# Optimization experiments

Measured on AMD Instinct MI355X. Metric: run time of the kernel, lower is better.

Reference implementation:

```python
import jax, jax.numpy as jnp
import numpy as np

N = 100000      # nodes
E = 1600000     # edges (avg degree 16)
D = 64          # in_channels == conv widths == lin width
G = 64          # graphs in batch
OUT = 10        # out_channels


def setup_inputs() -> dict:
    key = jax.random.key(0)
    ks = jax.random.split(key, 20)
    s = 0.1
    inp = {
        "x": jax.random.normal(ks[0], (N, D), jnp.float32),
        "edge_index": jax.random.randint(ks[1], (2, E), 0, N, dtype=jnp.int64),
        "batch": jnp.sort(jax.random.randint(ks[2], (N,), 0, G, dtype=jnp.int64)),
    }
    k = 3
    for i in range(3):  # 3 SAGEConv layers: lin_l (Wl, bl) on aggregated, lin_r (Wr, no bias) on root
        inp[f"c{i}_Wl"] = jax.random.normal(ks[k], (D, D), jnp.float32) * s; k += 1
        inp[f"c{i}_bl"] = jnp.zeros((D,), jnp.float32)
        inp[f"c{i}_Wr"] = jax.random.normal(ks[k], (D, D), jnp.float32) * s; k += 1
    inp["l0_W"] = jax.random.normal(ks[k], (D, D), jnp.float32) * s; k += 1
    inp["l0_b"] = jnp.zeros((D,), jnp.float32)
    inp["out_W"] = jax.random.normal(ks[k], (D, OUT), jnp.float32) * s; k += 1
    inp["out_b"] = jnp.zeros((OUT,), jnp.float32)
    return inp


def reference(x, edge_index, batch,
              c0_Wl, c0_bl, c0_Wr,
              c1_Wl, c1_bl, c1_Wr,
              c2_Wl, c2_bl, c2_Wr,
              l0_W, l0_b, out_W, out_b):
    src, dst = edge_index[0], edge_index[1]
    # in-degree of each target node (mean conv aggregation), computed once
    deg = jax.ops.segment_sum(jnp.ones((E,), x.dtype), dst, num_segments=N)
    inv_deg = (1.0 / jnp.maximum(deg, 1.0))[:, None]

    def sage(h, Wl, bl, Wr):
        # gather source features, mean-aggregate at targets, then lin_l(agg) + lin_r(h)
        agg = jax.ops.segment_sum(h[src], dst, num_segments=N) * inv_deg
        return agg @ Wl + bl + h @ Wr

    h = jax.nn.relu(sage(x, c0_Wl, c0_bl, c0_Wr))
    h = jax.nn.relu(sage(h, c1_Wl, c1_bl, c1_Wr))
    h = jax.nn.relu(sage(h, c2_Wl, c2_bl, c2_Wr))

    # global mean pool over graphs
    cnt = jax.ops.segment_sum(jnp.ones((N,), h.dtype), batch, num_segments=G)
    g = jax.ops.segment_sum(h, batch, num_segments=G) / jnp.maximum(cnt, 1.0)[:, None]

    g = jax.nn.relu(g @ l0_W + l0_b)
    return g @ out_W + out_b  # [G, OUT]
```

## Files before the change

kernel.cpp:

```cpp
#include <hip/hip_runtime.h>
#include <hip/hip_fp16.h>

#define WPB 8
#define PADK 136
#define BSH 8
#define BNODES 256
#define SC_BLOCKS 256
#define HIST_BLOCKS 256
#define HSTRIDE 512

typedef _Float16 half8 __attribute__((ext_vector_type(8)));
typedef _Float16 half4v __attribute__((ext_vector_type(4)));
typedef float floatx4 __attribute__((ext_vector_type(4)));

__global__ __launch_bounds__(256) void gnn_pre(const int* __restrict__ dst,
                                               int* __restrict__ bkt_cnt, int nbkt, int E,
                                               const int* __restrict__ batch,
                                               float* __restrict__ gcnt, int N,
                                               const float4* __restrict__ xin,
                                               ushort4* __restrict__ x16o, int n4,
                                               __half* __restrict__ x16,
                                               __half* __restrict__ hA,
                                               __half* __restrict__ hB,
                                               int* __restrict__ hist_all) {
    int tid = threadIdx.x;
    if (blockIdx.x < HIST_BLOCKS) {
        __shared__ int h[512];
        __shared__ int gb[64];
        for (int i = tid; i < nbkt; i += 256) h[i] = 0;
        if (tid < 64) gb[tid] = 0;
        __syncthreads();
        const int stride = HIST_BLOCKS * 256;
        if ((E & 3) == 0) {
            const int4* dst4 = (const int4*)dst;
            int E4 = E >> 2;
            for (int e = blockIdx.x * 256 + tid; e < E4; e += stride) {
                int4 d = dst4[e];
                atomicAdd(&h[d.x >> BSH], 1);
                atomicAdd(&h[d.y >> BSH], 1);
                atomicAdd(&h[d.z >> BSH], 1);
                atomicAdd(&h[d.w >> BSH], 1);
            }
        } else {
            for (int e = blockIdx.x * 256 + tid; e < E; e += stride)
                atomicAdd(&h[dst[e] >> BSH], 1);
        }
        for (int i = blockIdx.x * 256 + tid; i < N; i += stride)
            atomicAdd(&gb[batch[i]], 1);
        __syncthreads();
        for (int i = tid; i < nbkt; i += 256) {
            int v = h[i];
            hist_all[blockIdx.x * HSTRIDE + i] = v;
            if (v) atomicAdd(&bkt_cnt[i], v);
        }
        if (tid < 64) {
            int v = gb[tid];
            if (v) atomicAdd(&gcnt[tid], (float)v);
        }
        if (blockIdx.x == 0 && tid < 64) {
            x16[(size_t)N * 64 + tid] = __ushort_as_half((unsigned short)0);
            hA[(size_t)N * 64 + tid] = __ushort_as_half((unsigned short)0);
            hB[(size_t)N * 64 + tid] = __ushort_as_half((unsigned short)0);
        }
    } else {
        int i = (blockIdx.x - HIST_BLOCKS) * 256 + tid;
        if (i < n4) {
            float4 f = xin[i];
            ushort4 o;
            o.x = __half_as_ushort(__float2half(f.x));
            o.y = __half_as_ushort(__float2half(f.y));
            o.z = __half_as_ushort(__float2half(f.z));
            o.w = __half_as_ushort(__float2half(f.w));
            x16o[i] = o;
        }
    }
}

__global__ __launch_bounds__(256) void gnn_scan2(const int* __restrict__ hist_all,
                                                 const int* __restrict__ bkt_cnt,
                                                 int* __restrict__ bkt_base,
                                                 int* __restrict__ row_ptr,
                                                 int* __restrict__ blk_base_all,
                                                 int nbkt, int N) {
    int b = blockIdx.x;
    int t = threadIdx.x, lane = t & 63, wv = t >> 6;
    __shared__ int wsum[4];
    __shared__ int red[4];
    int part = 0;
    for (int i = t; i < b; i += 256) part += bkt_cnt[i];
#pragma unroll
    for (int off = 1; off < 64; off <<= 1) part += __shfl_xor(part, off);
    if (lane == 0) red[wv] = part;
    int v = hist_all[t * HSTRIDE + b];
    int x = v;
#pragma unroll
    for (int off = 1; off < 64; off <<= 1) {
        int y = __shfl_up(x, off);
        if (lane >= off) x += y;
    }
    if (lane == 63) wsum[wv] = x;
    __syncthreads();
    int base = red[0] + red[1] + red[2] + red[3];
    int wexcl = 0;
    for (int w = 0; w < wv; w++) wexcl += wsum[w];
    blk_base_all[t * HSTRIDE + b] = base + wexcl + (x - v);
    if (t == 0) {
        bkt_base[b] = base;
        if (b == nbkt - 1) {
            int tot = base + bkt_cnt[b];
            bkt_base[nbkt] = tot;
            row_ptr[N] = tot;
        }
    }
}

__global__ __launch_bounds__(256) void gnn_bkt_scatter(const int* __restrict__ src,
                                                       const int* __restrict__ dst,
                                                       const int* __restrict__ blk_base_all,
                                                       unsigned int* __restrict__ pairs,
                                                       int E, int nbkt) {
    __shared__ int cur[512];
    int tid = threadIdx.x;
    for (int i = tid; i < nbkt; i += 256) cur[i] = blk_base_all[blockIdx.x * HSTRIDE + i];
    __syncthreads();
    const int stride = SC_BLOCKS * 256;
    if ((E & 3) == 0) {
        const int4* dst4 = (const int4*)dst;
        const int4* src4 = (const int4*)src;
        int E4 = E >> 2;
        for (int e = blockIdx.x * 256 + tid; e < E4; e += stride) {
            int4 d = dst4[e];
            int4 s = src4[e];
            int p0 = atomicAdd(&cur[d.x >> BSH], 1);
            pairs[p0] = (unsigned int)s.x | ((unsigned int)(d.x & (BNODES - 1)) << 24);
            int p1 = atomicAdd(&cur[d.y >> BSH], 1);
            pairs[p1] = (unsigned int)s.y | ((unsigned int)(d.y & (BNODES - 1)) << 24);
            int p2 = atomicAdd(&cur[d.z >> BSH], 1);
            pairs[p2] = (unsigned int)s.z | ((unsigned int)(d.z & (BNODES - 1)) << 24);
            int p3 = atomicAdd(&cur[d.w >> BSH], 1);
            pairs[p3] = (unsigned int)s.w | ((unsigned int)(d.w & (BNODES - 1)) << 24);
        }
    } else {
        for (int e = blockIdx.x * 256 + tid; e < E; e += stride) {
            int d = dst[e];
            int b = d >> BSH;
            int p = atomicAdd(&cur[b], 1);
            pairs[p] = (unsigned int)src[e] | ((unsigned int)(d & (BNODES - 1)) << 24);
        }
    }
}

__global__ __launch_bounds__(256) void gnn_bkt_csr(const unsigned int* __restrict__ pairs,
                                                   const int* __restrict__ bkt_base,
                                                   int* __restrict__ row_ptr,
                                                   float* __restrict__ inv_deg,
                                                   int* __restrict__ csr_src, int N) {
    __shared__ int hist[BNODES];
    __shared__ int excl[BNODES];
    __shared__ int cur[BNODES];
    int b = blockIdx.x;
    int base = bkt_base[b];
    int cnt = bkt_base[b + 1] - base;
    int nd0 = b << BSH;
    int tid = threadIdx.x;
    hist[tid] = 0;
    __syncthreads();
    {
        int a0 = (4 - (base & 3)) & 3;
        a0 = min(a0, cnt);
        for (int i = tid; i < a0; i += 256) atomicAdd(&hist[pairs[base + i] >> 24], 1);
        int vcnt = (cnt - a0) >> 2;
        const uint4* p4 = (const uint4*)(pairs + base + a0);
        for (int i = tid; i < vcnt; i += 256) {
            uint4 u = p4[i];
            atomicAdd(&hist[u.x >> 24], 1);
            atomicAdd(&hist[u.y >> 24], 1);
            atomicAdd(&hist[u.z >> 24], 1);
            atomicAdd(&hist[u.w >> 24], 1);
        }
        for (int i = a0 + (vcnt << 2) + tid; i < cnt; i += 256)
            atomicAdd(&hist[pairs[base + i] >> 24], 1);
    }
    __syncthreads();
    if (tid < 64) {
        int carry = 0;
#pragma unroll
        for (int c = 0; c < BNODES; c += 64) {
            int v = hist[c + tid];
            int x = v;
#pragma unroll
            for (int off = 1; off < 64; off <<= 1) {
                int y = __shfl_up(x, off);
                if (tid >= off) x += y;
            }
            excl[c + tid] = carry + (x - v);
            carry += __shfl(x, 63);
        }
    }
    __syncthreads();
    {
        int node = nd0 + tid;
        if (node < N) {
            row_ptr[node] = base + excl[tid];
            int d = hist[tid];
            inv_deg[node] = 1.0f / (float)(d > 1 ? d : 1);
        }
        cur[tid] = excl[tid];
    }
    __syncthreads();
    {
        int a0 = (4 - (base & 3)) & 3;
        a0 = min(a0, cnt);
        for (int i = tid; i < a0; i += 256) {
            unsigned int u = pairs[base + i];
            int pos = atomicAdd(&cur[u >> 24], 1);
            csr_src[base + pos] = (int)(u & 0xFFFFFFu);
        }
        int vcnt = (cnt - a0) >> 2;
        const uint4* p4 = (const uint4*)(pairs + base + a0);
        for (int i = tid; i < vcnt; i += 256) {
            uint4 u = p4[i];
            int pos0 = atomicAdd(&cur[u.x >> 24], 1);
            csr_src[base + pos0] = (int)(u.x & 0xFFFFFFu);
            int pos1 = atomicAdd(&cur[u.y >> 24], 1);
            csr_src[base + pos1] = (int)(u.y & 0xFFFFFFu);
            int pos2 = atomicAdd(&cur[u.z >> 24], 1);
            csr_src[base + pos2] = (int)(u.z & 0xFFFFFFu);
            int pos3 = atomicAdd(&cur[u.w >> 24], 1);
            csr_src[base + pos3] = (int)(u.w & 0xFFFFFFu);
        }
        for (int i = a0 + (vcnt << 2) + tid; i < cnt; i += 256) {
            unsigned int u = pairs[base + i];
            int pos = atomicAdd(&cur[u >> 24], 1);
            csr_src[base + pos] = (int)(u & 0xFFFFFFu);
        }
    }
}

#define LOAD4(eReg, c0, vArr)                                  \
    _Pragma("unroll") for (int c_ = 0; c_ < 4; c_++) {         \
        int sj_ = __shfl(eReg, (c0) + c_ * 4 + quad);          \
        vArr[c_] = hin4v[(size_t)sj_ * 16 + m16];              \
    }
#define ACC4(vArr, accum)                                      \
    _Pragma("unroll") for (int c_ = 0; c_ < 4; c_++) {         \
        accum.x += (float)vArr[c_][0];                         \
        accum.y += (float)vArr[c_][1];                         \
        accum.z += (float)vArr[c_][2];                         \
        accum.w += (float)vArr[c_][3];                         \
    }

__global__ __launch_bounds__(512, 4) void gnn_sage(const __half* __restrict__ hin,
                                                   __half* __restrict__ hout,
                                                   const int* __restrict__ row_ptr,
                                                   const int* __restrict__ csr_src,
                                                   const float* __restrict__ inv_deg,
                                                   const float* __restrict__ Wl,
                                                   const float* __restrict__ bl,
                                                   const float* __restrict__ Wr, int n) {
    __shared__ _Float16 w_lds[64 * PADK];
    __shared__ _Float16 in_lds[WPB][16 * PADK];
    int tid = threadIdx.x, lane = tid & 63, wv = tid >> 6;
    for (int i = tid; i < 64 * 64; i += 512) {
        int k = i >> 6, nn = i & 63;
        w_lds[nn * PADK + k] = (_Float16)Wl[i];
        w_lds[nn * PADK + 64 + k] = (_Float16)Wr[i];
    }
    __syncthreads();
    int ngroups = (n + 15) >> 4;
    int g = blockIdx.x * WPB + wv;
    if (g >= ngroups) return;
    int m16 = lane & 15, quad = lane >> 4;
    int hf = lane >> 5, col = lane & 31;
    float bias[4];
#pragma unroll
    for (int nt = 0; nt < 4; nt++) bias[nt] = bl[nt * 16 + m16];
    _Float16* my_in = in_lds[wv];
    const unsigned* hin32 = (const unsigned*)hin;
    const half4v* hin4v = (const half4v*)hin;
    int nd0 = g << 4;
    int nclamp = n - 1 - nd0;
    int idx = nd0 + lane;
    int rr = (lane <= 16) ? row_ptr[min(idx, n)] : 0;
    float ig = (lane < 16) ? inv_deg[min(idx, n - 1)] : 0.0f;

#pragma unroll
    for (int jp = 0; jp < 8; jp++) {
        int j2 = jp << 1;
        int nd = nd0 + min(j2 + hf, nclamp);
        unsigned u = hin32[(size_t)nd * 32 + col];
        ((unsigned*)(my_in + (j2 + hf) * PADK + 64))[col] = u;
    }

    int ef[16];
#pragma unroll
    for (int j = 0; j < 16; j++) {
        int jj = min(j, nclamp);
        int s0 = __shfl(rr, jj), s1 = __shfl(rr, jj + 1);
        int cb = min(64, s1 - s0);
        ef[j] = (lane < cb) ? csr_src[s0 + lane] : n;
    }

#pragma unroll
    for (int jp = 0; jp < 8; jp++) {
        int j2 = jp << 1;
        int jjA = min(j2, nclamp), jjB = min(j2 + 1, nclamp);
        int s0A = __shfl(rr, jjA), s1A = __shfl(rr, jjA + 1);
        int s0B = __shfl(rr, jjB), s1B = __shfl(rr, jjB + 1);
        float idgA = __shfl(ig, jjA), idgB = __shfl(ig, jjB);
        int cbA = min(64, s1A - s0A), cbB = min(64, s1B - s0B);
        floatx4 accA = {0.f, 0.f, 0.f, 0.f};
        floatx4 accB = {0.f, 0.f, 0.f, 0.f};
        {
            half4v vA[4], vB[4];
            LOAD4(ef[j2], 0, vA);
            LOAD4(ef[j2 + 1], 0, vB);
            ACC4(vA, accA);
            ACC4(vB, accB);
        }
        if (cbA > 16) {
            half4v v0[4];
            LOAD4(ef[j2], 16, v0);
            ACC4(v0, accA);
            if (cbA > 32) { half4v v1[4]; LOAD4(ef[j2], 32, v1); ACC4(v1, accA); }
            if (cbA > 48) { half4v v2[4]; LOAD4(ef[j2], 48, v2); ACC4(v2, accA); }
        }
        if (cbB > 16) {
            half4v v0[4];
            LOAD4(ef[j2 + 1], 16, v0);
            ACC4(v0, accB);
            if (cbB > 32) { half4v v1[4]; LOAD4(ef[j2 + 1], 32, v1); ACC4(v1, accB); }
            if (cbB > 48) { half4v v2[4]; LOAD4(ef[j2 + 1], 48, v2); ACC4(v2, accB); }
        }
        for (int base_ = s0A + 64; base_ < s1A; base_ += 64) {
            int cb = min(64, s1A - base_);
            int ei = (lane < cb) ? csr_src[base_ + lane] : n;
            for (int i0 = 0; i0 < cb; i0 += 16) {
                half4v vt[4];
                LOAD4(ei, i0, vt);
                ACC4(vt, accA);
            }
        }
        for (int base_ = s0B + 64; base_ < s1B; base_ += 64) {
            int cb = min(64, s1B - base_);
            int ei = (lane < cb) ? csr_src[base_ + lane] : n;
            for (int i0 = 0; i0 < cb; i0 += 16) {
                half4v vt[4];
                LOAD4(ei, i0, vt);
                ACC4(vt, accB);
            }
        }
        accA.x += __shfl_xor(accA.x, 16); accA.y += __shfl_xor(accA.y, 16);
        accA.z += __shfl_xor(accA.z, 16); accA.w += __shfl_xor(accA.w, 16);
        accA.x += __shfl_xor(accA.x, 32); accA.y += __shfl_xor(accA.y, 32);
        accA.z += __shfl_xor(accA.z, 32); accA.w += __shfl_xor(accA.w, 32);
        accB.x += __shfl_xor(accB.x, 16); accB.y += __shfl_xor(accB.y, 16);
        accB.z += __shfl_xor(accB.z, 16); accB.w += __shfl_xor(accB.w, 16);
        accB.x += __shfl_xor(accB.x, 32); accB.y += __shfl_xor(accB.y, 32);
        accB.z += __shfl_xor(accB.z, 32); accB.w += __shfl_xor(accB.w, 32);
        if (quad == 0) {
            half4v hw;
            hw[0] = (_Float16)(accA.x * idgA);
            hw[1] = (_Float16)(accA.y * idgA);
            hw[2] = (_Float16)(accA.z * idgA);
            hw[3] = (_Float16)(accA.w * idgA);
            *(half4v*)(my_in + j2 * PADK + m16 * 4) = hw;
        } else if (quad == 1) {
            half4v hw;
            hw[0] = (_Float16)(accB.x * idgB);
            hw[1] = (_Float16)(accB.y * idgB);
            hw[2] = (_Float16)(accB.z * idgB);
            hw[3] = (_Float16)(accB.w * idgB);
            *(half4v*)(my_in + (j2 + 1) * PADK + m16 * 4) = hw;
        }
    }
    half8 afrag[4];
    const _Float16* abase = my_in + m16 * PADK + quad * 8;
#pragma unroll
    for (int ks = 0; ks < 4; ks++) afrag[ks] = *(const half8*)(abase + ks * 32);
    floatx4 accv[4];
#pragma unroll
    for (int nt = 0; nt < 4; nt++) {
        accv[nt].x = 0.f; accv[nt].y = 0.f; accv[nt].z = 0.f; accv[nt].w = 0.f;
    }
#pragma unroll
    for (int nt = 0; nt < 4; nt++) {
        const _Float16* bbase = w_lds + (nt * 16 + m16) * PADK + quad * 8;
#pragma unroll
        for (int ks = 0; ks < 4; ks++) {
            half8 bfrag = *(const half8*)(bbase + ks * 32);
            accv[nt] = __builtin_amdgcn_mfma_f32_16x16x32_f16(afrag[ks], bfrag, accv[nt], 0, 0, 0);
        }
    }
#pragma unroll
    for (int nt = 0; nt < 4; nt++) {
#pragma unroll
        for (int r = 0; r < 4; r++) {
            int node = nd0 + quad * 4 + r;
            if (node < n) {
                float v = fmaxf(accv[nt][r] + bias[nt], 0.0f);
                hout[(size_t)node * 64 + nt * 16 + m16] = __float2half(v);
            }
        }
    }
}

__global__ __launch_bounds__(512, 4) void gnn_sage_pool(const __half* __restrict__ hin,
                                                        const int* __restrict__ row_ptr,
                                                        const int* __restrict__ csr_src,
                                                        const float* __restrict__ inv_deg,
                                                        const float* __restrict__ Wl,
                                                        const float* __restrict__ bl,
                                                        const float* __restrict__ Wr,
                                                        const int* __restrict__ batch,
                                                        float* __restrict__ gsum,
                                                        const float* __restrict__ gcnt,
                                                        const float* __restrict__ l0W,
                                                        const float* __restrict__ l0b,
                                                        const float* __restrict__ outW,
                                                        const float* __restrict__ outb,
                                                        float* __restrict__ out,
                                                        unsigned int* __restrict__ done,
                                                        int G, int OUT, int n) {
    __shared__ _Float16 w_lds[64 * PADK];
    __shared__ _Float16 in_lds[WPB][16 * PADK];
    __shared__ int lastsh;
    int tid = threadIdx.x, lane = tid & 63, wv = tid >> 6;
    for (int i = tid; i < 64 * 64; i += 512) {
        int k = i >> 6, nn = i & 63;
        w_lds[nn * PADK + k] = (_Float16)Wl[i];
        w_lds[nn * PADK + 64 + k] = (_Float16)Wr[i];
    }
    __syncthreads();
    int ngroups = (n + 15) >> 4;
    int g = blockIdx.x * WPB + wv;
    int m16 = lane & 15, quad = lane >> 4;
    int hf = lane >> 5, col = lane & 31;
    const unsigned* hin32 = (const unsigned*)hin;
    const half4v* hin4v = (const half4v*)hin;
    if (g < ngroups) {
        float bias[4];
#pragma unroll
        for (int nt = 0; nt < 4; nt++) bias[nt] = bl[nt * 16 + m16];
        _Float16* my_in = in_lds[wv];
        int nd0 = g << 4;
        int nclamp = n - 1 - nd0;
        int idx = nd0 + lane;
        int rr = (lane <= 16) ? row_ptr[min(idx, n)] : 0;
        float ig = (lane < 16) ? inv_deg[min(idx, n - 1)] : 0.0f;

#pragma unroll
        for (int jp = 0; jp < 8; jp++) {
            int j2 = jp << 1;
            int nd = nd0 + min(j2 + hf, nclamp);
            unsigned u = hin32[(size_t)nd * 32 + col];
            ((unsigned*)(my_in + (j2 + hf) * PADK + 64))[col] = u;
        }

        int ef[16];
#pragma unroll
        for (int j = 0; j < 16; j++) {
            int jj = min(j, nclamp);
            int s0 = __shfl(rr, jj), s1 = __shfl(rr, jj + 1);
            int cb = min(64, s1 - s0);
            ef[j] = (lane < cb) ? csr_src[s0 + lane] : n;
        }

#pragma unroll
        for (int jp = 0; jp < 8; jp++) {
            int j2 = jp << 1;
            int jjA = min(j2, nclamp), jjB = min(j2 + 1, nclamp);
            int s0A = __shfl(rr, jjA), s1A = __shfl(rr, jjA + 1);
            int s0B = __shfl(rr, jjB), s1B = __shfl(rr, jjB + 1);
            float idgA = __shfl(ig, jjA), idgB = __shfl(ig, jjB);
            int cbA = min(64, s1A - s0A), cbB = min(64, s1B - s0B);
            floatx4 accA = {0.f, 0.f, 0.f, 0.f};
            floatx4 accB = {0.f, 0.f, 0.f, 0.f};
            {
                half4v vA[4], vB[4];
                LOAD4(ef[j2], 0, vA);
                LOAD4(ef[j2 + 1], 0, vB);
                ACC4(vA, accA);
                ACC4(vB, accB);
            }
            if (cbA > 16) {
                half4v v0[4];
                LOAD4(ef[j2], 16, v0);
                ACC4(v0, accA);
                if (cbA > 32) { half4v v1[4]; LOAD4(ef[j2], 32, v1); ACC4(v1, accA); }
                if (cbA > 48) { half4v v2[4]; LOAD4(ef[j2], 48, v2); ACC4(v2, accA); }
            }
            if (cbB > 16) {
                half4v v0[4];
                LOAD4(ef[j2 + 1], 16, v0);
                ACC4(v0, accB);
                if (cbB > 32) { half4v v1[4]; LOAD4(ef[j2 + 1], 32, v1); ACC4(v1, accB); }
                if (cbB > 48) { half4v v2[4]; LOAD4(ef[j2 + 1], 48, v2); ACC4(v2, accB); }
            }
            for (int base_ = s0A + 64; base_ < s1A; base_ += 64) {
                int cb = min(64, s1A - base_);
                int ei = (lane < cb) ? csr_src[base_ + lane] : n;
                for (int i0 = 0; i0 < cb; i0 += 16) {
                    half4v vt[4];
                    LOAD4(ei, i0, vt);
                    ACC4(vt, accA);
                }
            }
            for (int base_ = s0B + 64; base_ < s1B; base_ += 64) {
                int cb = min(64, s1B - base_);
                int ei = (lane < cb) ? csr_src[base_ + lane] : n;
                for (int i0 = 0; i0 < cb; i0 += 16) {
                    half4v vt[4];
                    LOAD4(ei, i0, vt);
                    ACC4(vt, accB);
                }
            }
            accA.x += __shfl_xor(accA.x, 16); accA.y += __shfl_xor(accA.y, 16);
            accA.z += __shfl_xor(accA.z, 16); accA.w += __shfl_xor(accA.w, 16);
            accA.x += __shfl_xor(accA.x, 32); accA.y += __shfl_xor(accA.y, 32);
            accA.z += __shfl_xor(accA.z, 32); accA.w += __shfl_xor(accA.w, 32);
            accB.x += __shfl_xor(accB.x, 16); accB.y += __shfl_xor(accB.y, 16);
            accB.z += __shfl_xor(accB.z, 16); accB.w += __shfl_xor(accB.w, 16);
            accB.x += __shfl_xor(accB.x, 32); accB.y += __shfl_xor(accB.y, 32);
            accB.z += __shfl_xor(accB.z, 32); accB.w += __shfl_xor(accB.w, 32);
            if (quad == 0) {
                half4v hw;
                hw[0] = (_Float16)(accA.x * idgA);
                hw[1] = (_Float16)(accA.y * idgA);
                hw[2] = (_Float16)(accA.z * idgA);
                hw[3] = (_Float16)(accA.w * idgA);
                *(half4v*)(my_in + j2 * PADK + m16 * 4) = hw;
            } else if (quad == 1) {
                half4v hw;
                hw[0] = (_Float16)(accB.x * idgB);
                hw[1] = (_Float16)(accB.y * idgB);
                hw[2] = (_Float16)(accB.z * idgB);
                hw[3] = (_Float16)(accB.w * idgB);
                *(half4v*)(my_in + (j2 + 1) * PADK + m16 * 4) = hw;
            }
        }
        half8 afrag[4];
        const _Float16* abase = my_in + m16 * PADK + quad * 8;
#pragma unroll
        for (int ks = 0; ks < 4; ks++) afrag[ks] = *(const half8*)(abase + ks * 32);
        floatx4 accv[4];
#pragma unroll
        for (int nt = 0; nt < 4; nt++) {
            accv[nt].x = 0.f; accv[nt].y = 0.f; accv[nt].z = 0.f; accv[nt].w = 0.f;
        }
#pragma unroll
        for (int nt = 0; nt < 4; nt++) {
            const _Float16* bbase = w_lds + (nt * 16 + m16) * PADK + quad * 8;
#pragma unroll
            for (int ks = 0; ks < 4; ks++) {
                half8 bfrag = *(const half8*)(bbase + ks * 32);
                accv[nt] = __builtin_amdgcn_mfma_f32_16x16x32_f16(afrag[ks], bfrag, accv[nt], 0, 0, 0);
            }
        }
        int bFirst = batch[nd0];
        int bLast = batch[min(nd0 + 15, n - 1)];
        if (bFirst == bLast && nd0 + 15 < n) {
#pragma unroll
            for (int nt = 0; nt < 4; nt++) {
                float s = fmaxf(accv[nt][0] + bias[nt], 0.0f) + fmaxf(accv[nt][1] + bias[nt], 0.0f) +
                          fmaxf(accv[nt][2] + bias[nt], 0.0f) + fmaxf(accv[nt][3] + bias[nt], 0.0f);
                s += __shfl_xor(s, 16);
                s += __shfl_xor(s, 32);
                if (quad == 0) atomicAdd(&gsum[bFirst * 64 + nt * 16 + m16], s);
            }
        } else {
#pragma unroll
            for (int nt = 0; nt < 4; nt++) {
#pragma unroll
                for (int r = 0; r < 4; r++) {
                    int node = nd0 + quad * 4 + r;
                    if (node < n) {
                        int bg = batch[node];
                        float v = fmaxf(accv[nt][r] + bias[nt], 0.0f);
                        atomicAdd(&gsum[bg * 64 + nt * 16 + m16], v);
                    }
                }
            }
        }
    }
    __syncthreads();
    if (tid == 0) {
        __threadfence();
        unsigned int old = atomicAdd(done, 1u);
        lastsh = (old == gridDim.x - 1) ? 1 : 0;
    }
    __syncthreads();
    if (lastsh) {
        float* gm = (float*)&in_lds[0][0];
        float* t2 = gm + 64 * 64;
        for (int i = tid; i < G * 64; i += 512) {
            int r = i >> 6;
            float s = atomicAdd(&gsum[i], 0.0f);
            gm[i] = s / fmaxf(gcnt[r], 1.0f);
        }
        __syncthreads();
        for (int i = tid; i < G * 64; i += 512) {
            int r = i >> 6, c = i & 63;
            float s = l0b[c];
#pragma unroll 8
            for (int k = 0; k < 64; k++) s += gm[(r << 6) + k] * l0W[(k << 6) + c];
            t2[i] = fmaxf(s, 0.0f);
        }
        __syncthreads();
        for (int i = tid; i < G * OUT; i += 512) {
            int r = i / OUT, c = i - r * OUT;
            float s = outb[c];
#pragma unroll 8
            for (int k = 0; k < 64; k++) s += t2[(r << 6) + k] * outW[k * OUT + c];
            out[i] = s;
        }
    }
}

extern "C" void kernel_launch(void* const* d_in, const int* in_sizes, int n_in,
                              void* d_out, int out_size, void* d_ws, size_t ws_size,
                              hipStream_t stream) {
    const float* x = (const float*)d_in[0];
    const int* ei = (const int*)d_in[1];
    const int* batch = (const int*)d_in[2];
    const float* Wl[3] = {(const float*)d_in[3], (const float*)d_in[6], (const float*)d_in[9]};
    const float* bl[3] = {(const float*)d_in[4], (const float*)d_in[7], (const float*)d_in[10]};
    const float* Wr[3] = {(const float*)d_in[5], (const float*)d_in[8], (const float*)d_in[11]};
    const float* l0W = (const float*)d_in[12];
    const float* l0b = (const float*)d_in[13];
    const float* outW = (const float*)d_in[14];
    const float* outb = (const float*)d_in[15];

    int N = in_sizes[2];
    int E = in_sizes[1] / 2;
    int OUT = 10;
    int G = out_size / OUT;
    const int* src = ei;
    const int* dst = ei + E;
    int NBKT = (N + BNODES - 1) >> BSH;

    char* ws = (char*)d_ws;
    size_t off = 0;
    auto alloc = [&](size_t b) -> char* {
        char* p = ws + off;
        off = (off + b + 255) & ~(size_t)255;
        return p;
    };
    int* row_ptr = (int*)alloc((size_t)(N + 1) * 4);
    int* csr_src = (int*)alloc((size_t)E * 4);
    float* inv_deg = (float*)alloc((size_t)N * 4);
    size_t zoff = off;
    int* bkt_cnt = (int*)alloc((size_t)NBKT * 4);
    float* gcnt = (float*)alloc((size_t)G * 4);
    float* gsum = (float*)alloc((size_t)G * 64 * 4);
    unsigned int* done = (unsigned int*)alloc(4);
    size_t zlen = off - zoff;
    int* bkt_base = (int*)alloc((size_t)(NBKT + 1) * 4);
    int* hist_all = (int*)alloc((size_t)HIST_BLOCKS * HSTRIDE * 4);
    int* blk_base_all = (int*)alloc((size_t)HIST_BLOCKS * HSTRIDE * 4);
    unsigned int* pairs = (unsigned int*)alloc((size_t)E * 4);
    __half* x16 = (__half*)alloc((size_t)(N + 1) * 64 * 2);
    __half* hA = (__half*)alloc((size_t)(N + 1) * 64 * 2);
    __half* hB = (__half*)alloc((size_t)(N + 1) * 64 * 2);

    hipMemsetAsync(ws + zoff, 0, zlen, stream);

    int n4 = N * 64 / 4;
    int pre_blocks = HIST_BLOCKS + (n4 + 255) / 256;
    gnn_pre<<<pre_blocks, 256, 0, stream>>>(dst, bkt_cnt, NBKT, E, batch, gcnt, N,
                                            (const float4*)x, (ushort4*)x16, n4,
                                            x16, hA, hB, hist_all);
    gnn_scan2<<<NBKT, 256, 0, stream>>>(hist_all, bkt_cnt, bkt_base, row_ptr,
                                        blk_base_all, NBKT, N);
    gnn_bkt_scatter<<<SC_BLOCKS, 256, 0, stream>>>(src, dst, blk_base_all, pairs, E, NBKT);
    gnn_bkt_csr<<<NBKT, 256, 0, stream>>>(pairs, bkt_base, row_ptr, inv_deg, csr_src, N);

    int ngroups = (N + 15) >> 4;
    int sage_blocks = (ngroups + WPB - 1) / WPB;
    gnn_sage<<<sage_blocks, 512, 0, stream>>>(x16, hA, row_ptr, csr_src, inv_deg,
                                              Wl[0], bl[0], Wr[0], N);
    gnn_sage<<<sage_blocks, 512, 0, stream>>>(hA, hB, row_ptr, csr_src, inv_deg,
                                              Wl[1], bl[1], Wr[1], N);
    gnn_sage_pool<<<sage_blocks, 512, 0, stream>>>(hB, row_ptr, csr_src, inv_deg,
                                                   Wl[2], bl[2], Wr[2], batch, gsum,
                                                   gcnt, l0W, l0b, outW, outb,
                                                   (float*)d_out, done, G, OUT, N);
}
```

Baseline: 304.5 us.

## Stage bucket pairs in LDS for CSR build and split pooling head into own kernel

The bucket CSR kernel now copies each bucket's packed pairs into a 48KB shared-memory buffer during the histogram pass. The scatter pass reads them from LDS instead of re-reading global memory, and it drops the uint4-vectorized global loads. Separately, the last-block-done atomic counter and tail MLP head are removed from the final SAGE/pool kernel and moved to a separate single-block head kernel. This lets waves with no work exit early and removes the threadfence and atomic handshake. The cost is an extra kernel launch, and the large LDS buffer may lower occupancy in the CSR kernel.

```diff
diff --git a/kernel.cpp b/kernel.cpp
--- a/kernel.cpp
+++ b/kernel.cpp
@@ -8,6 +8,7 @@
 #define SC_BLOCKS 256
 #define HIST_BLOCKS 256
 #define HSTRIDE 512
+#define PSTAGE 12288
 
 typedef _Float16 half8 __attribute__((ext_vector_type(8)));
 typedef _Float16 half4v __attribute__((ext_vector_type(4)));
@@ -158,6 +159,7 @@
     __shared__ int hist[BNODES];
     __shared__ int excl[BNODES];
     __shared__ int cur[BNODES];
+    __shared__ unsigned int pstage[PSTAGE];
     int b = blockIdx.x;
     int base = bkt_base[b];
     int cnt = bkt_base[b + 1] - base;
@@ -165,22 +167,14 @@
     int tid = threadIdx.x;
     hist[tid] = 0;
     __syncthreads();
-    {
-        int a0 = (4 - (base & 3)) & 3;
-        a0 = min(a0, cnt);
-        for (int i = tid; i < a0; i += 256) atomicAdd(&hist[pairs[base + i] >> 24], 1);
-        int vcnt = (cnt - a0) >> 2;
-        const uint4* p4 = (const uint4*)(pairs + base + a0);
-        for (int i = tid; i < vcnt; i += 256) {
-            uint4 u = p4[i];
-            atomicAdd(&hist[u.x >> 24], 1);
-            atomicAdd(&hist[u.y >> 24], 1);
-            atomicAdd(&hist[u.z >> 24], 1);
-            atomicAdd(&hist[u.w >> 24], 1);
-        }
-        for (int i = a0 + (vcnt << 2) + tid; i < cnt; i += 256)
-            atomicAdd(&hist[pairs[base + i] >> 24], 1);
-    }
+    int scnt = min(cnt, PSTAGE);
+    for (int i = tid; i < scnt; i += 256) {
+        unsigned int u = pairs[base + i];
+        pstage[i] = u;
+        atomicAdd(&hist[u >> 24], 1);
+    }
+    for (int i = scnt + tid; i < cnt; i += 256)
+        atomicAdd(&hist[pairs[base + i] >> 24], 1);
     __syncthreads();
     if (tid < 64) {
         int carry = 0;
@@ -208,32 +202,15 @@
         cur[tid] = excl[tid];
     }
     __syncthreads();
-    {
-        int a0 = (4 - (base & 3)) & 3;
-        a0 = min(a0, cnt);
-        for (int i = tid; i < a0; i += 256) {
-            unsigned int u = pairs[base + i];
-            int pos = atomicAdd(&cur[u >> 24], 1);
-            csr_src[base + pos] = (int)(u & 0xFFFFFFu);
-        }
-        int vcnt = (cnt - a0) >> 2;
-        const uint4* p4 = (const uint4*)(pairs + base + a0);
-        for (int i = tid; i < vcnt; i += 256) {
-            uint4 u = p4[i];
-            int pos0 = atomicAdd(&cur[u.x >> 24], 1);
-            csr_src[base + pos0] = (int)(u.x & 0xFFFFFFu);
-            int pos1 = atomicAdd(&cur[u.y >> 24], 1);
-            csr_src[base + pos1] = (int)(u.y & 0xFFFFFFu);
-            int pos2 = atomicAdd(&cur[u.z >> 24], 1);
-            csr_src[base + pos2] = (int)(u.z & 0xFFFFFFu);
-            int pos3 = atomicAdd(&cur[u.w >> 24], 1);
-            csr_src[base + pos3] = (int)(u.w & 0xFFFFFFu);
-        }
-        for (int i = a0 + (vcnt << 2) + tid; i < cnt; i += 256) {
-            unsigned int u = pairs[base + i];
-            int pos = atomicAdd(&cur[u >> 24], 1);
-            csr_src[base + pos] = (int)(u & 0xFFFFFFu);
-        }
+    for (int i = tid; i < scnt; i += 256) {
+        unsigned int u = pstage[i];
+        int pos = atomicAdd(&cur[u >> 24], 1);
+        csr_src[base + pos] = (int)(u & 0xFFFFFFu);
+    }
+    for (int i = scnt + tid; i < cnt; i += 256) {
+        unsigned int u = pairs[base + i];
+        int pos = atomicAdd(&cur[u >> 24], 1);
+        csr_src[base + pos] = (int)(u & 0xFFFFFFu);
     }
 }
 
@@ -413,18 +390,9 @@
                                                         const float* __restrict__ bl,
                                                         const float* __restrict__ Wr,
                                                         const int* __restrict__ batch,
-                                                        float* __restrict__ gsum,
-                                                        const float* __restrict__ gcnt,
-                                                        const float* __restrict__ l0W,
-                                                        const float* __restrict__ l0b,
-                                                        const float* __restrict__ outW,
-                                                        const float* __restrict__ outb,
-                                                        float* __restrict__ out,
-                                                        unsigned int* __restrict__ done,
-                                                        int G, int OUT, int n) {
+                                                        float* __restrict__ gsum, int n) {
     __shared__ _Float16 w_lds[64 * PADK];
     __shared__ _Float16 in_lds[WPB][16 * PADK];
-    __shared__ int lastsh;
     int tid = threadIdx.x, lane = tid & 63, wv = tid >> 6;
     for (int i = tid; i < 64 * 64; i += 512) {
         int k = i >> 6, nn = i & 63;
@@ -434,186 +402,185 @@
     __syncthreads();
     int ngroups = (n + 15) >> 4;
     int g = blockIdx.x * WPB + wv;
+    if (g >= ngroups) return;
     int m16 = lane & 15, quad = lane >> 4;
     int hf = lane >> 5, col = lane & 31;
+    float bias[4];
+#pragma unroll
+    for (int nt = 0; nt < 4; nt++) bias[nt] = bl[nt * 16 + m16];
+    _Float16* my_in = in_lds[wv];
     const unsigned* hin32 = (const unsigned*)hin;
     const half4v* hin4v = (const half4v*)hin;
-    if (g < ngroups) {
-        float bias[4];
-#pragma unroll
-        for (int nt = 0; nt < 4; nt++) bias[nt] = bl[nt * 16 + m16];
-        _Float16* my_in = in_lds[wv];
-        int nd0 = g << 4;
-        int nclamp = n - 1 - nd0;
-        int idx = nd0 + lane;
-        int rr = (lane <= 16) ? row_ptr[min(idx, n)] : 0;
-        float ig = (lane < 16) ? inv_deg[min(idx, n - 1)] : 0.0f;
-
-#pragma unroll
-        for (int jp = 0; jp < 8; jp++) {
-            int j2 = jp << 1;
-            int nd = nd0 + min(j2 + hf, nclamp);
-            unsigned u = hin32[(size_t)nd * 32 + col];
-            ((unsigned*)(my_in + (j2 + hf) * PADK + 64))[col] = u;
-        }
-
-        int ef[16];
-#pragma unroll
-        for (int j = 0; j < 16; j++) {
-            int jj = min(j, nclamp);
-            int s0 = __shfl(rr, jj), s1 = __shfl(rr, jj + 1);
-            int cb = min(64, s1 - s0);
-            ef[j] = (lane < cb) ? csr_src[s0 + lane] : n;
-        }
-
-#pragma unroll
-        for (int jp = 0; jp < 8; jp++) {
-            int j2 = jp << 1;
-            int jjA = min(j2, nclamp), jjB = min(j2 + 1, nclamp);
-            int s0A = __shfl(rr, jjA), s1A = __shfl(rr, jjA + 1);
-            int s0B = __shfl(rr, jjB), s1B = __shfl(rr, jjB + 1);
-            float idgA = __shfl(ig, jjA), idgB = __shfl(ig, jjB);
-            int cbA = min(64, s1A - s0A), cbB = min(64, s1B - s0B);
-            floatx4 accA = {0.f, 0.f, 0.f, 0.f};
-            floatx4 accB = {0.f, 0.f, 0.f, 0.f};
-            {
-                half4v vA[4], vB[4];
-                LOAD4(ef[j2], 0, vA);
-                LOAD4(ef[j2 + 1], 0, vB);
-                ACC4(vA, accA);
-                ACC4(vB, accB);
-            }
-            if (cbA > 16) {
-                half4v v0[4];
-                LOAD4(ef[j2], 16, v0);
-                ACC4(v0, accA);
-                if (cbA > 32) { half4v v1[4]; LOAD4(ef[j2], 32, v1); ACC4(v1, accA); }
-                if (cbA > 48) { half4v v2[4]; LOAD4(ef[j2], 48, v2); ACC4(v2, accA); }
-            }
-            if (cbB > 16) {
-                half4v v0[4];
-                LOAD4(ef[j2 + 1], 16, v0);
-                ACC4(v0, accB);
-                if (cbB > 32) { half4v v1[4]; LOAD4(ef[j2 + 1], 32, v1); ACC4(v1, accB); }
-                if (cbB > 48) { half4v v2[4]; LOAD4(ef[j2 + 1], 48, v2); ACC4(v2, accB); }
-            }
-            for (int base_ = s0A + 64; base_ < s1A; base_ += 64) {
-                int cb = min(64, s1A - base_);
-                int ei = (lane < cb) ? csr_src[base_ + lane] : n;
-                for (int i0 = 0; i0 < cb; i0 += 16) {
-                    half4v vt[4];
-                    LOAD4(ei, i0, vt);
-                    ACC4(vt, accA);
+    int nd0 = g << 4;
+    int nclamp = n - 1 - nd0;
+    int idx = nd0 + lane;
+    int rr = (lane <= 16) ? row_ptr[min(idx, n)] : 0;
+    float ig = (lane < 16) ? inv_deg[min(idx, n - 1)] : 0.0f;
+
+#pragma unroll
+    for (int jp = 0; jp < 8; jp++) {
+        int j2 = jp << 1;
+        int nd = nd0 + min(j2 + hf, nclamp);
+        unsigned u = hin32[(size_t)nd * 32 + col];
+        ((unsigned*)(my_in + (j2 + hf) * PADK + 64))[col] = u;
+    }
+
+    int ef[16];
+#pragma unroll
+    for (int j = 0; j < 16; j++) {
+        int jj = min(j, nclamp);
+        int s0 = __shfl(rr, jj), s1 = __shfl(rr, jj + 1);
+        int cb = min(64, s1 - s0);
+        ef[j] = (lane < cb) ? csr_src[s0 + lane] : n;
+    }
+
+#pragma unroll
+    for (int jp = 0; jp < 8; jp++) {
+        int j2 = jp << 1;
+        int jjA = min(j2, nclamp), jjB = min(j2 + 1, nclamp);
+        int s0A = __shfl(rr, jjA), s1A = __shfl(rr, jjA + 1);
+        int s0B = __shfl(rr, jjB), s1B = __shfl(rr, jjB + 1);
+        float idgA = __shfl(ig, jjA), idgB = __shfl(ig, jjB);
+        int cbA = min(64, s1A - s0A), cbB = min(64, s1B - s0B);
+        floatx4 accA = {0.f, 0.f, 0.f, 0.f};
+        floatx4 accB = {0.f, 0.f, 0.f, 0.f};
+        {
+            half4v vA[4], vB[4];
+            LOAD4(ef[j2], 0, vA);
+            LOAD4(ef[j2 + 1], 0, vB);
+            ACC4(vA, accA);
+            ACC4(vB, accB);
+        }
+        if (cbA > 16) {
+            half4v v0[4];
+            LOAD4(ef[j2], 16, v0);
+            ACC4(v0, accA);
+            if (cbA > 32) { half4v v1[4]; LOAD4(ef[j2], 32, v1); ACC4(v1, accA); }
+            if (cbA > 48) { half4v v2[4]; LOAD4(ef[j2], 48, v2); ACC4(v2, accA); }
+        }
+        if (cbB > 16) {
+            half4v v0[4];
+            LOAD4(ef[j2 + 1], 16, v0);
+            ACC4(v0, accB);
+            if (cbB > 32) { half4v v1[4]; LOAD4(ef[j2 + 1], 32, v1); ACC4(v1, accB); }
+            if (cbB > 48) { half4v v2[4]; LOAD4(ef[j2 + 1], 48, v2); ACC4(v2, accB); }
+        }
+        for (int base_ = s0A + 64; base_ < s1A; base_ += 64) {
+            int cb = min(64, s1A - base_);
+            int ei = (lane < cb) ? csr_src[base_ + lane] : n;
+            for (int i0 = 0; i0 < cb; i0 += 16) {
+                half4v vt[4];
+                LOAD4(ei, i0, vt);
+                ACC4(vt, accA);
+            }
+        }
+        for (int base_ = s0B + 64; base_ < s1B; base_ += 64) {
+            int cb = min(64, s1B - base_);
+            int ei = (lane < cb) ? csr_src[base_ + lane] : n;
+            for (int i0 = 0; i0 < cb; i0 += 16) {
+                half4v vt[4];
+                LOAD4(ei, i0, vt);
+                ACC4(vt, accB);
+            }
+        }
+        accA.x += __shfl_xor(accA.x, 16); accA.y += __shfl_xor(accA.y, 16);
+        accA.z += __shfl_xor(accA.z, 16); accA.w += __shfl_xor(accA.w, 16);
+        accA.x += __shfl_xor(accA.x, 32); accA.y += __shfl_xor(accA.y, 32);
+        accA.z += __shfl_xor(accA.z, 32); accA.w += __shfl_xor(accA.w, 32);
+        accB.x += __shfl_xor(accB.x, 16); accB.y += __shfl_xor(accB.y, 16);
+        accB.z += __shfl_xor(accB.z, 16); accB.w += __shfl_xor(accB.w, 16);
+        accB.x += __shfl_xor(accB.x, 32); accB.y += __shfl_xor(accB.y, 32);
+        accB.z += __shfl_xor(accB.z, 32); accB.w += __shfl_xor(accB.w, 32);
+        if (quad == 0) {
+            half4v hw;
+            hw[0] = (_Float16)(accA.x * idgA);
+            hw[1] = (_Float16)(accA.y * idgA);
+            hw[2] = (_Float16)(accA.z * idgA);
+            hw[3] = (_Float16)(accA.w * idgA);
+            *(half4v*)(my_in + j2 * PADK + m16 * 4) = hw;
+        } else if (quad == 1) {
+            half4v hw;
+            hw[0] = (_Float16)(accB.x * idgB);
+            hw[1] = (_Float16)(accB.y * idgB);
+            hw[2] = (_Float16)(accB.z * idgB);
+            hw[3] = (_Float16)(accB.w * idgB);
+            *(half4v*)(my_in + (j2 + 1) * PADK + m16 * 4) = hw;
+        }
+    }
+    half8 afrag[4];
+    const _Float16* abase = my_in + m16 * PADK + quad * 8;
+#pragma unroll
+    for (int ks = 0; ks < 4; ks++) afrag[ks] = *(const half8*)(abase + ks * 32);
+    floatx4 accv[4];
+#pragma unroll
+    for (int nt = 0; nt < 4; nt++) {
+        accv[nt].x = 0.f; accv[nt].y = 0.f; accv[nt].z = 0.f; accv[nt].w = 0.f;
+    }
+#pragma unroll
+    for (int nt = 0; nt < 4; nt++) {
+        const _Float16* bbase = w_lds + (nt * 16 + m16) * PADK + quad * 8;
+#pragma unroll
+        for (int ks = 0; ks < 4; ks++) {
+            half8 bfrag = *(const half8*)(bbase + ks * 32);
+            accv[nt] = __builtin_amdgcn_mfma_f32_16x16x32_f16(afrag[ks], bfrag, accv[nt], 0, 0, 0);
+        }
+    }
+    int bFirst = batch[nd0];
+    int bLast = batch[min(nd0 + 15, n - 1)];
+    if (bFirst == bLast && nd0 + 15 < n) {
+#pragma unroll
+        for (int nt = 0; nt < 4; nt++) {
+            float s = fmaxf(accv[nt][0] + bias[nt], 0.0f) + fmaxf(accv[nt][1] + bias[nt], 0.0f) +
+                      fmaxf(accv[nt][2] + bias[nt], 0.0f) + fmaxf(accv[nt][3] + bias[nt], 0.0f);
+            s += __shfl_xor(s, 16);
+            s += __shfl_xor(s, 32);
+            if (quad == 0) atomicAdd(&gsum[bFirst * 64 + nt * 16 + m16], s);
+        }
+    } else {
+#pragma unroll
+        for (int nt = 0; nt < 4; nt++) {
+#pragma unroll
+            for (int r = 0; r < 4; r++) {
+                int node = nd0 + quad * 4 + r;
+                if (node < n) {
+                    int bg = batch[node];
+                    float v = fmaxf(accv[nt][r] + bias[nt], 0.0f);
+                    atomicAdd(&gsum[bg * 64 + nt * 16 + m16], v);
                 }
             }
-            for (int base_ = s0B + 64; base_ < s1B; base_ += 64) {
-                int cb = min(64, s1B - base_);
-                int ei = (lane < cb) ? csr_src[base_ + lane] : n;
-                for (int i0 = 0; i0 < cb; i0 += 16) {
-                    half4v vt[4];
-                    LOAD4(ei, i0, vt);
-                    ACC4(vt, accB);
-                }
-            }
-            accA.x += __shfl_xor(accA.x, 16); accA.y += __shfl_xor(accA.y, 16);
-            accA.z += __shfl_xor(accA.z, 16); accA.w += __shfl_xor(accA.w, 16);
-            accA.x += __shfl_xor(accA.x, 32); accA.y += __shfl_xor(accA.y, 32);
-            accA.z += __shfl_xor(accA.z, 32); accA.w += __shfl_xor(accA.w, 32);
-            accB.x += __shfl_xor(accB.x, 16); accB.y += __shfl_xor(accB.y, 16);
-            accB.z += __shfl_xor(accB.z, 16); accB.w += __shfl_xor(accB.w, 16);
-            accB.x += __shfl_xor(accB.x, 32); accB.y += __shfl_xor(accB.y, 32);
-            accB.z += __shfl_xor(accB.z, 32); accB.w += __shfl_xor(accB.w, 32);
-            if (quad == 0) {
-                half4v hw;
-                hw[0] = (_Float16)(accA.x * idgA);
-                hw[1] = (_Float16)(accA.y * idgA);
-                hw[2] = (_Float16)(accA.z * idgA);
-                hw[3] = (_Float16)(accA.w * idgA);
-                *(half4v*)(my_in + j2 * PADK + m16 * 4) = hw;
-            } else if (quad == 1) {
-                half4v hw;
-                hw[0] = (_Float16)(accB.x * idgB);
-                hw[1] = (_Float16)(accB.y * idgB);
-                hw[2] = (_Float16)(accB.z * idgB);
-                hw[3] = (_Float16)(accB.w * idgB);
-                *(half4v*)(my_in + (j2 + 1) * PADK + m16 * 4) = hw;
-            }
-        }
-        half8 afrag[4];
-        const _Float16* abase = my_in + m16 * PADK + quad * 8;
-#pragma unroll
-        for (int ks = 0; ks < 4; ks++) afrag[ks] = *(const half8*)(abase + ks * 32);
-        floatx4 accv[4];
-#pragma unroll
-        for (int nt = 0; nt < 4; nt++) {
-            accv[nt].x = 0.f; accv[nt].y = 0.f; accv[nt].z = 0.f; accv[nt].w = 0.f;
-        }
-#pragma unroll
-        for (int nt = 0; nt < 4; nt++) {
-            const _Float16* bbase = w_lds + (nt * 16 + m16) * PADK + quad * 8;
-#pragma unroll
-            for (int ks = 0; ks < 4; ks++) {
-                half8 bfrag = *(const half8*)(bbase + ks * 32);
-                accv[nt] = __builtin_amdgcn_mfma_f32_16x16x32_f16(afrag[ks], bfrag, accv[nt], 0, 0, 0);
-            }
-        }
-        int bFirst = batch[nd0];
-        int bLast = batch[min(nd0 + 15, n - 1)];
-        if (bFirst == bLast && nd0 + 15 < n) {
-#pragma unroll
-            for (int nt = 0; nt < 4; nt++) {
-                float s = fmaxf(accv[nt][0] + bias[nt], 0.0f) + fmaxf(accv[nt][1] + bias[nt], 0.0f) +
-                          fmaxf(accv[nt][2] + bias[nt], 0.0f) + fmaxf(accv[nt][3] + bias[nt], 0.0f);
-                s += __shfl_xor(s, 16);
-                s += __shfl_xor(s, 32);
-                if (quad == 0) atomicAdd(&gsum[bFirst * 64 + nt * 16 + m16], s);
-            }
-        } else {
-#pragma unroll
-            for (int nt = 0; nt < 4; nt++) {
-#pragma unroll
-                for (int r = 0; r < 4; r++) {
-                    int node = nd0 + quad * 4 + r;
-                    if (node < n) {
-                        int bg = batch[node];
-                        float v = fmaxf(accv[nt][r] + bias[nt], 0.0f);
-                        atomicAdd(&gsum[bg * 64 + nt * 16 + m16], v);
-                    }
-                }
-            }
-        }
-    }
-    __syncthreads();
-    if (tid == 0) {
-        __threadfence();
-        unsigned int old = atomicAdd(done, 1u);
-        lastsh = (old == gridDim.x - 1) ? 1 : 0;
-    }
-    __syncthreads();
-    if (lastsh) {
-        float* gm = (float*)&in_lds[0][0];
-        float* t2 = gm + 64 * 64;
-        for (int i = tid; i < G * 64; i += 512) {
-            int r = i >> 6;
-            float s = atomicAdd(&gsum[i], 0.0f);
-            gm[i] = s / fmaxf(gcnt[r], 1.0f);
-        }
-        __syncthreads();
-        for (int i = tid; i < G * 64; i += 512) {
-            int r = i >> 6, c = i & 63;
-            float s = l0b[c];
+        }
+    }
+}
+
+__global__ __launch_bounds__(1024) void gnn_head(const float* __restrict__ gsum,
+                                                 const float* __restrict__ gcnt,
+                                                 const float* __restrict__ l0W,
+                                                 const float* __restrict__ l0b,
+                                                 const float* __restrict__ outW,
+                                                 const float* __restrict__ outb,
+                                                 float* __restrict__ out, int G, int OUT) {
+    __shared__ float gm[64 * 64];
+    __shared__ float t2[64 * 64];
+    int tid = threadIdx.x;
+    for (int i = tid; i < G * 64; i += 1024) {
+        int r = i >> 6;
+        gm[i] = gsum[i] / fmaxf(gcnt[r], 1.0f);
+    }
+    __syncthreads();
+    for (int i = tid; i < G * 64; i += 1024) {
+        int r = i >> 6, c = i & 63;
+        float s = l0b[c];
 #pragma unroll 8
-            for (int k = 0; k < 64; k++) s += gm[(r << 6) + k] * l0W[(k << 6) + c];
-            t2[i] = fmaxf(s, 0.0f);
-        }
-        __syncthreads();
-        for (int i = tid; i < G * OUT; i += 512) {
-            int r = i / OUT, c = i - r * OUT;
-            float s = outb[c];
+        for (int k = 0; k < 64; k++) s += gm[(r << 6) + k] * l0W[(k << 6) + c];
+        t2[i] = fmaxf(s, 0.0f);
+    }
+    __syncthreads();
+    for (int i = tid; i < G * OUT; i += 1024) {
+        int r = i / OUT, c = i - r * OUT;
+        float s = outb[c];
 #pragma unroll 8
-            for (int k = 0; k < 64; k++) s += t2[(r << 6) + k] * outW[k * OUT + c];
-            out[i] = s;
-        }
+        for (int k = 0; k < 64; k++) s += t2[(r << 6) + k] * outW[k * OUT + c];
+        out[i] = s;
     }
 }
 
@@ -653,7 +620,6 @@
     int* bkt_cnt = (int*)alloc((size_t)NBKT * 4);
     float* gcnt = (float*)alloc((size_t)G * 4);
     float* gsum = (float*)alloc((size_t)G * 64 * 4);
-    unsigned int* done = (unsigned int*)alloc(4);
     size_t zlen = off - zoff;
     int* bkt_base = (int*)alloc((size_t)(NBKT + 1) * 4);
     int* hist_all = (int*)alloc((size_t)HIST_BLOCKS * HSTRIDE * 4);
@@ -682,7 +648,7 @@
     gnn_sage<<<sage_blocks, 512, 0, stream>>>(hA, hB, row_ptr, csr_src, inv_deg,
                                               Wl[1], bl[1], Wr[1], N);
     gnn_sage_pool<<<sage_blocks, 512, 0, stream>>>(hB, row_ptr, csr_src, inv_deg,
-                                                   Wl[2], bl[2], Wr[2], batch, gsum,
-                                                   gcnt, l0W, l0b, outW, outb,
-                                                   (float*)d_out, done, G, OUT, N);
-}
+                                                   Wl[2], bl[2], Wr[2], batch, gsum, N);
+
+    gnn_head<<<1, 1024, 0, stream>>>(gsum, gcnt, l0W, l0b, outW, outb, (float*)d_out, G, OUT);
+}
```

After: 291.8 us, median of 3. -4.2%, faster.
